# Kernel tuning notes

Hardware: AMD Instinct MI355X
Metric: run time of the kernel (lower is better)

Reference implementation:

```python
import jax, jax.numpy as jnp
import numpy as np


def _xcorr3x3_valid(x, k):
    # x: [B,H,W], k: [B,3,3] per-sample kernel; cross-correlation (matches F.conv2d), VALID padding
    B, H, W = x.shape
    out = jnp.zeros((B, H - 2, W - 2), dtype=x.dtype)
    for u in range(3):
        for v in range(3):
            out = out + x[:, u:u + H - 2, v:v + W - 2] * k[:, u, v, None, None]
    return out


def setup_inputs() -> dict:
    key = jax.random.key(0)
    ks = jax.random.split(key, 4)
    B, H, W = 256, 256, 256
    pred = jax.random.normal(ks[0], (B, H, W), dtype=jnp.float32)
    rhs = jax.random.normal(ks[1], (B, H - 2, W - 2), dtype=jnp.float32)
    Laplace_kernel = jax.random.normal(ks[2], (B, 3, 3), dtype=jnp.float32)
    Df_dr_kernel = jax.random.normal(ks[3], (B, 3, 3), dtype=jnp.float32)
    # physically sensible meshgrids: R in [1,2] (avoids div-by-zero), Z in [-1,1]
    r = jnp.linspace(1.0, 2.0, W, dtype=jnp.float32)
    z = jnp.linspace(-1.0, 1.0, H, dtype=jnp.float32)
    RR = jnp.broadcast_to(r[None, None, :], (B, H, W)).astype(jnp.float32)
    ZZ = jnp.broadcast_to(z[None, :, None], (B, H, W)).astype(jnp.float32)
    Gauss_kernel = (jnp.array([[1., 2., 1.], [2., 4., 2.], [1., 2., 1.]], dtype=jnp.float32) / 16.0)
    return {"pred": pred, "rhs": rhs, "Laplace_kernel": Laplace_kernel,
            "Df_dr_kernel": Df_dr_kernel, "RR": RR, "ZZ": ZZ, "Gauss_kernel": Gauss_kernel}


def reference(pred, rhs, Laplace_kernel, Df_dr_kernel, RR, ZZ, Gauss_kernel):
    # Lpsi, Dpsi_dr: per-sample 3x3 VALID stencils -> [B, H-2, W-2]
    Lpsi = _xcorr3x3_valid(pred, Laplace_kernel)
    Dpsi_dr = -_xcorr3x3_valid(pred, Df_dr_kernel)
    Dpsi_dr = Dpsi_dr / RR[:, 1:-1, 1:-1]
    lhs = Lpsi - Dpsi_dr
    hr = (RR[:, 1, 2] - RR[:, 1, 1])[:, None, None]
    hz = (ZZ[:, 2, 1] - ZZ[:, 1, 1])[:, None, None]
    alfa = -2.0 * (hr ** 2 + hz ** 2)
    GS_ope = lhs * alfa / (hr ** 2 * hz ** 2)
    # Gaussian smoothing, shared kernel, SAME padding (cross-correlation; kernel is symmetric)
    sm = jax.lax.conv_general_dilated(
        GS_ope[:, None, :, :], Gauss_kernel[None, None, :, :],
        window_strides=(1, 1), padding='SAME')
    GS_ope_smooth = -sm
    rhs_computed = -GS_ope_smooth[:, 0, :, :]
    return jnp.mean((rhs_computed - rhs) ** 2)
```

## Files before the change

### kernel.cpp

```cpp
#include <hip/hip_runtime.h>


#define STRIP 32

__global__ __launch_bounds__(256, 8)
void pde_loss_kernel(const float* __restrict__ pred,
                     const float* __restrict__ rhs,
                     const float* __restrict__ KL,
                     const float* __restrict__ KD,
                     const float* __restrict__ RR,
                     const float* __restrict__ ZZ,
                     float* __restrict__ out,
                     float inv_n)
{
    constexpr int H = 256, W = 256, OH = 254, OW = 254;
    const int tid   = threadIdx.x;
    const int strip = blockIdx.x & 7;
    const int b     = blockIdx.x >> 3;
    const int o0 = strip * STRIP;
    const int o1 = (o0 + STRIP < OH) ? (o0 + STRIP) : OH;

    __shared__ float spred[3][W];
    __shared__ float gsbuf[W];

    const size_t ib   = (size_t)b * H * W;
    const float* predb = pred + ib;
    const float* rhsb  = rhs + (size_t)b * OH * OW;

    const float hr  = RR[ib + W + 2] - RR[ib + W + 1];
    const float hz  = ZZ[ib + 2 * W + 1] - ZZ[ib + W + 1];
    const float hr2 = hr * hr, hz2 = hz * hz;
    const float s   = -2.0f * (hr2 + hz2) / (hr2 * hz2);

    float coef[9];
    {
        float inv_r = 0.0f;
        if (tid < OW) inv_r = 1.0f / RR[ib + W + (tid + 1)];
        const float* kl = KL + b * 9;
        const float* kd = KD + b * 9;
#pragma unroll
        for (int t = 0; t < 9; ++t)
            coef[t] = (kl[t] + kd[t] * inv_r) * s;
    }

    const int g0 = o0 - 1;
    if (g0 >= 0) {
        if (tid < 64)
            ((float4*)spred[g0 % 3])[tid] = ((const float4*)(predb + (size_t)g0 * W))[tid];
    }
    if (tid < 64)
        ((float4*)spred[(g0 + 1) % 3])[tid] = ((const float4*)(predb + (size_t)(g0 + 1) * W))[tid];

    float ghA = 0.0f, ghB = 0.0f;
    float acc = 0.0f;

    for (int g = g0; g <= o1; ++g) {
        const int p = g + 2;
        if (p < H && tid < 64)
            ((float4*)spred[p % 3])[tid] = ((const float4*)(predb + (size_t)p * W))[tid];
        __syncthreads();

        float gs = 0.0f;
        if (g >= 0 && g < OH && tid < OW) {
            const float* r0 = spred[g % 3];
            const float* r1 = spred[(g + 1) % 3];
            const float* r2 = spred[(g + 2) % 3];
            gs = fmaf(r0[tid],     coef[0],
                 fmaf(r0[tid + 1], coef[1],
                 fmaf(r0[tid + 2], coef[2],
                 fmaf(r1[tid],     coef[3],
                 fmaf(r1[tid + 1], coef[4],
                 fmaf(r1[tid + 2], coef[5],
                 fmaf(r2[tid],     coef[6],
                 fmaf(r2[tid + 1], coef[7],
                      r2[tid + 2] * coef[8]))))))));
        }
        if (tid < OW)       gsbuf[tid + 1] = gs;
        else if (tid == OW) gsbuf[0]   = 0.0f;
        else                gsbuf[W-1] = 0.0f;
        __syncthreads();

        float ghC = 0.0f;
        if (tid < OW)
            ghC = gsbuf[tid] + 2.0f * gsbuf[tid + 1] + gsbuf[tid + 2];

        const int i = g - 1;
        if (i >= o0 && i < o1 && tid < OW) {
            const float sm = (ghA + 2.0f * ghB + ghC) * 0.0625f;
            const float d  = sm - rhsb[(size_t)i * OW + tid];
            acc = fmaf(d, d, acc);
        }
        ghA = ghB; ghB = ghC;
    }

#pragma unroll
    for (int off = 32; off > 0; off >>= 1)
        acc += __shfl_down(acc, off, 64);
    __shared__ float wsum[4];
    if ((tid & 63) == 0) wsum[tid >> 6] = acc;
    __syncthreads();
    if (tid == 0) {
        const float t = (wsum[0] + wsum[1]) + (wsum[2] + wsum[3]);
        atomicAdd(out, t * inv_n);
    }
}

extern "C" void kernel_launch(void* const* d_in, const int* in_sizes, int n_in,
                              void* d_out, int out_size, void* d_ws, size_t ws_size,
                              hipStream_t stream) {
    const float* pred = (const float*)d_in[0];
    const float* rhs  = (const float*)d_in[1];
    const float* KL   = (const float*)d_in[2];
    const float* KD   = (const float*)d_in[3];
    const float* RR   = (const float*)d_in[4];
    const float* ZZ   = (const float*)d_in[5];
    float* out = (float*)d_out;

    const int B = in_sizes[2] / 9;
    const float inv_n = 1.0f / ((float)B * 254.0f * 254.0f);

    hipMemsetAsync(out, 0, sizeof(float), stream);
    pde_loss_kernel<<<dim3(B * 8), dim3(256), 0, stream>>>(pred, rhs, KL, KD, RR, ZZ, out, inv_n);
}
```

Measured before the change: 246.9 us.

## Map each wavefront to a row strip with register stencils and shuffles

Each 64-lane wavefront now owns a 16-row strip, and each lane handles 4 adjacent columns through float4 loads. Shared-memory row buffers and per-row __syncthreads are replaced by a rolling window of register rows, with horizontal neighbours and the horizontal Gaussian pass exchanged by wavefront shuffles. The rhs row is prefetched one iteration ahead. This is meant to remove block-wide barriers and LDS traffic, at the cost of more registers per thread (launch bounds lowered to 4 blocks) and two extra halo rows loaded per 16-row strip.

New measurement: 223.6 us. 1.1x faster.

```diff
diff --git a/kernel.cpp b/kernel.cpp
--- a/kernel.cpp
+++ b/kernel.cpp
@@ -1,9 +1,7 @@
 #include <hip/hip_runtime.h>
 
 
-#define STRIP 32
-
-__global__ __launch_bounds__(256, 8)
+__global__ __launch_bounds__(256, 4)
 void pde_loss_kernel(const float* __restrict__ pred,
                      const float* __restrict__ rhs,
                      const float* __restrict__ KL,
@@ -14,16 +12,15 @@
                      float inv_n)
 {
     constexpr int H = 256, W = 256, OH = 254, OW = 254;
-    const int tid   = threadIdx.x;
-    const int strip = blockIdx.x & 7;
-    const int b     = blockIdx.x >> 3;
-    const int o0 = strip * STRIP;
-    const int o1 = (o0 + STRIP < OH) ? (o0 + STRIP) : OH;
+    const int tid = threadIdx.x;
+    const int l   = tid & 63;
+    const int wv  = tid >> 6;
+    const int b   = blockIdx.x >> 2;
+    const int strip = (blockIdx.x & 3) * 4 + wv;
+    const int o0 = strip * 16;
+    const int o1 = (o0 + 16 < OH) ? (o0 + 16) : OH;
 
-    __shared__ float spred[3][W];
-    __shared__ float gsbuf[W];
-
-    const size_t ib   = (size_t)b * H * W;
+    const size_t ib = (size_t)b * H * W;
     const float* predb = pred + ib;
     const float* rhsb  = rhs + (size_t)b * OH * OW;
 
@@ -32,72 +29,106 @@
     const float hr2 = hr * hr, hz2 = hz * hz;
     const float s   = -2.0f * (hr2 + hz2) / (hr2 * hz2);
 
-    float coef[9];
+    const int c0 = 4 * l;
+    float4 c4[9];
     {
-        float inv_r = 0.0f;
-        if (tid < OW) inv_r = 1.0f / RR[ib + W + (tid + 1)];
+        float4 invr;
+        invr.x = 1.0f / RR[ib + W + (c0 + 1)];
+        invr.y = 1.0f / RR[ib + W + (c0 + 2)];
+        invr.z = 1.0f / RR[ib + W + (c0 + 3)];
+        invr.w = 1.0f / RR[ib + W + ((c0 + 4 < W) ? (c0 + 4) : (W - 1))];
         const float* kl = KL + b * 9;
         const float* kd = KD + b * 9;
 #pragma unroll
-        for (int t = 0; t < 9; ++t)
-            coef[t] = (kl[t] + kd[t] * inv_r) * s;
+        for (int t = 0; t < 9; ++t) {
+            const float a = kl[t] * s, d = kd[t] * s;
+            c4[t].x = fmaf(d, invr.x, a);
+            c4[t].y = fmaf(d, invr.y, a);
+            c4[t].z = fmaf(d, invr.z, a);
+            c4[t].w = fmaf(d, invr.w, a);
+        }
     }
 
     const int g0 = o0 - 1;
-    if (g0 >= 0) {
-        if (tid < 64)
-            ((float4*)spred[g0 % 3])[tid] = ((const float4*)(predb + (size_t)g0 * W))[tid];
-    }
-    if (tid < 64)
-        ((float4*)spred[(g0 + 1) % 3])[tid] = ((const float4*)(predb + (size_t)(g0 + 1) * W))[tid];
+    float4 pa = make_float4(0.f, 0.f, 0.f, 0.f), pb, pc;
+    if (g0 >= 0) pa = *(const float4*)(predb + (size_t)g0 * W + c0);
+    pb = *(const float4*)(predb + (size_t)(g0 + 1) * W + c0);
+    pc = *(const float4*)(predb + (size_t)(g0 + 2) * W + c0);
+    float nxa = __shfl(pa.x, l + 1, 64), nya = __shfl(pa.y, l + 1, 64);
+    float nxb = __shfl(pb.x, l + 1, 64), nyb = __shfl(pb.y, l + 1, 64);
 
-    float ghA = 0.0f, ghB = 0.0f;
+    float4 ghA = make_float4(0.f, 0.f, 0.f, 0.f);
+    float4 ghB = make_float4(0.f, 0.f, 0.f, 0.f);
+    float2 rc0 = make_float2(0.f, 0.f), rc1 = make_float2(0.f, 0.f);
     float acc = 0.0f;
 
     for (int g = g0; g <= o1; ++g) {
-        const int p = g + 2;
-        if (p < H && tid < 64)
-            ((float4*)spred[p % 3])[tid] = ((const float4*)(predb + (size_t)p * W))[tid];
-        __syncthreads();
+        float4 pn = make_float4(0.f, 0.f, 0.f, 0.f);
+        const int rowp = g + 3;
+        if (rowp < H && rowp <= o1 + 2)
+            pn = *(const float4*)(predb + (size_t)rowp * W + c0);
 
-        float gs = 0.0f;
-        if (g >= 0 && g < OH && tid < OW) {
-            const float* r0 = spred[g % 3];
-            const float* r1 = spred[(g + 1) % 3];
-            const float* r2 = spred[(g + 2) % 3];
-            gs = fmaf(r0[tid],     coef[0],
-                 fmaf(r0[tid + 1], coef[1],
-                 fmaf(r0[tid + 2], coef[2],
-                 fmaf(r1[tid],     coef[3],
-                 fmaf(r1[tid + 1], coef[4],
-                 fmaf(r1[tid + 2], coef[5],
-                 fmaf(r2[tid],     coef[6],
-                 fmaf(r2[tid + 1], coef[7],
-                      r2[tid + 2] * coef[8]))))))));
+        float2 rn0 = make_float2(0.f, 0.f), rn1 = make_float2(0.f, 0.f);
+        if (g >= o0 && g < o1) {
+            const float* rrow = rhsb + (size_t)g * OW + c0;
+            rn0 = *(const float2*)rrow;
+            if (c0 + 2 < OW) rn1 = *(const float2*)(rrow + 2);
         }
-        if (tid < OW)       gsbuf[tid + 1] = gs;
-        else if (tid == OW) gsbuf[0]   = 0.0f;
-        else                gsbuf[W-1] = 0.0f;
-        __syncthreads();
 
-        float ghC = 0.0f;
-        if (tid < OW)
-            ghC = gsbuf[tid] + 2.0f * gsbuf[tid + 1] + gsbuf[tid + 2];
+        const float nxc = __shfl(pc.x, l + 1, 64);
+        const float nyc = __shfl(pc.y, l + 1, 64);
+
+        float4 gs = make_float4(0.f, 0.f, 0.f, 0.f);
+        if ((unsigned)g < (unsigned)OH) {
+#define ROWC(p, nx, ny, t0)                                              \
+            gs.x = fmaf(p.x, c4[t0].x, fmaf(p.y, c4[t0+1].x, fmaf(p.z, c4[t0+2].x, gs.x))); \
+            gs.y = fmaf(p.y, c4[t0].y, fmaf(p.z, c4[t0+1].y, fmaf(p.w, c4[t0+2].y, gs.y))); \
+            gs.z = fmaf(p.z, c4[t0].z, fmaf(p.w, c4[t0+1].z, fmaf(nx,  c4[t0+2].z, gs.z))); \
+            gs.w = fmaf(p.w, c4[t0].w, fmaf(nx,  c4[t0+1].w, fmaf(ny,  c4[t0+2].w, gs.w)));
+            ROWC(pa, nxa, nya, 0)
+            ROWC(pb, nxb, nyb, 3)
+            ROWC(pc, nxc, nyc, 6)
+#undef ROWC
+            if (l == 63) { gs.z = 0.f; gs.w = 0.f; }
+        }
+
+        float up = __shfl(gs.w, l - 1, 64);
+        const float dn = __shfl(gs.x, l + 1, 64);
+        if (l == 0) up = 0.f;
+        float4 gh;
+        gh.x = fmaf(2.f, gs.x, up   + gs.y);
+        gh.y = fmaf(2.f, gs.y, gs.x + gs.z);
+        gh.z = fmaf(2.f, gs.z, gs.y + gs.w);
+        gh.w = fmaf(2.f, gs.w, gs.z + dn);
 
         const int i = g - 1;
-        if (i >= o0 && i < o1 && tid < OW) {
-            const float sm = (ghA + 2.0f * ghB + ghC) * 0.0625f;
-            const float d  = sm - rhsb[(size_t)i * OW + tid];
-            acc = fmaf(d, d, acc);
+        if (i >= o0 && i < o1) {
+            const float smx = (ghA.x + 2.f * ghB.x + gh.x) * 0.0625f;
+            const float smy = (ghA.y + 2.f * ghB.y + gh.y) * 0.0625f;
+            const float smz = (ghA.z + 2.f * ghB.z + gh.z) * 0.0625f;
+            const float smw = (ghA.w + 2.f * ghB.w + gh.w) * 0.0625f;
+            const float dx = smx - rc0.x;
+            const float dy = smy - rc0.y;
+            float dz = smz - rc1.x;
+            float dw = smw - rc1.y;
+            if (c0 + 2 >= OW) { dz = 0.f; dw = 0.f; }
+            acc = fmaf(dx, dx, acc);
+            acc = fmaf(dy, dy, acc);
+            acc = fmaf(dz, dz, acc);
+            acc = fmaf(dw, dw, acc);
         }
-        ghA = ghB; ghB = ghC;
+
+        pa = pb; pb = pc; pc = pn;
+        nxa = nxb; nya = nyb; nxb = nxc; nyb = nyc;
+        ghA = ghB; ghB = gh;
+        rc0 = rn0; rc1 = rn1;
     }
 
 #pragma unroll
     for (int off = 32; off > 0; off >>= 1)
         acc += __shfl_down(acc, off, 64);
     __shared__ float wsum[4];
-    if ((tid & 63) == 0) wsum[tid >> 6] = acc;
+    if (l == 0) wsum[wv] = acc;
     __syncthreads();
     if (tid == 0) {
         const float t = (wsum[0] + wsum[1]) + (wsum[2] + wsum[3]);
@@ -120,5 +151,5 @@
     const float inv_n = 1.0f / ((float)B * 254.0f * 254.0f);
 
     hipMemsetAsync(out, 0, sizeof(float), stream);
-    pde_loss_kernel<<<dim3(B * 8), dim3(256), 0, stream>>>(pred, rhs, KL, KD, RR, ZZ, out, inv_n);
+    pde_loss_kernel<<<dim3(B * 4), dim3(256), 0, stream>>>(pred, rhs, KL, KD, RR, ZZ, out, inv_n);
 }
```
